# Kernel optimization log

Measured on AMD Instinct MI355X. Metric: run time of the kernel, lower is better.

The kernel has to match this reference:

```python
import jax, jax.numpy as jnp
import numpy as np

EYE_PENALTY = 1.0e6


def setup_inputs() -> dict:
    key = jax.random.key(0)
    k1, k2 = jax.random.split(key)
    B, NIN, NK, DK = 512, 1024, 128, 5
    x = jax.random.normal(k1, (B, NIN), dtype=jnp.float32)
    theta = jax.random.normal(k2, (NIN, NK, DK), dtype=jnp.float32) * 0.05
    log_weight_scale = jnp.zeros((NK, DK), dtype=jnp.float32)
    bias = jnp.full((NK,), -1.0, dtype=jnp.float32)
    return {"x": x, "theta": theta, "log_weight_scale": log_weight_scale, "bias": bias}


def reference(x, theta, log_weight_scale, bias):
    # kernel = theta * exp(log_weight_scale) / ||theta||_2 (norm over input dim)
    l2 = jnp.sqrt(jnp.sum(theta * theta, axis=0))            # [K, D]
    kernel = theta * (jnp.exp(log_weight_scale) / l2)[None]   # [NIN, K, D]
    actv = jnp.einsum('bi,ikd->bkd', x, kernel)               # [B, K, D]
    B = x.shape[0]
    # all-pairs L1 distance per kernel: [B, K, B]
    diff = actv[:, :, :, None] - jnp.transpose(actv, (1, 2, 0))[None]  # [B,K,D,B]
    abs_dif = jnp.sum(jnp.abs(diff), axis=2)                  # [B, K, B]
    abs_dif = abs_dif + EYE_PENALTY * jnp.eye(B, dtype=x.dtype)[:, None, :]
    f = jnp.sum(jnp.exp(-abs_dif), axis=2) + bias[None, :]    # [B, K]
    return jnp.concatenate([x, f], axis=1)                    # [B, NIN + K]
```

## Files before the change

### kernel.cpp

```cpp
#include <hip/hip_runtime.h>
#include <hip/hip_fp16.h>
#include <math.h>

constexpr int B    = 512;
constexpr int NIN  = 1024;
constexpr int NK   = 128;
constexpr int DK   = 5;
constexpr int NF   = NK * DK;
constexpr int NOUT = NIN + NK;
constexpr int SPLITK = 8;
constexpr int LDA = 136;
#define LOG2E 1.44269504088896f

typedef _Float16 f16x4 __attribute__((ext_vector_type(4)));
typedef _Float16 f16x8 __attribute__((ext_vector_type(8)));
typedef float    f32x4 __attribute__((ext_vector_type(4)));

union H2 { __half2 h; unsigned u; };

__global__ __launch_bounds__(256) void gemm_kernel(
        const float* __restrict__ x,
        const float* __restrict__ theta,
        __half* __restrict__ actvP16,
        float* __restrict__ ps) {
    __shared__ _Float16 Ath[32 * LDA];
    __shared__ _Float16 Bxh[64 * LDA];
    __shared__ float    red2[32][33];

    const int t    = threadIdx.x;
    const int tile = blockIdx.x >> 3;
    const int z    = blockIdx.x & 7;
    const int nt   = tile >> 3;
    const int bt   = tile & 7;
    const int n0   = nt * 32;
    const int b0   = bt * 64;
    const bool do_ps = (bt == 0);
    const int kw   = z * 128;

    const int kq = t >> 3;
    const int nc = (t & 7) * 4;
    float4 tv0 = *(const float4*)&theta[(kw + kq*4 + 0) * NF + n0 + nc];
    float4 tv1 = *(const float4*)&theta[(kw + kq*4 + 1) * NF + n0 + nc];
    float4 tv2 = *(const float4*)&theta[(kw + kq*4 + 2) * NF + n0 + nc];
    float4 tv3 = *(const float4*)&theta[(kw + kq*4 + 3) * NF + n0 + nc];

    const int br = t >> 2;
    const int ki = t & 3;
    float4 xv[8];
    #pragma unroll
    for (int i = 0; i < 8; ++i)
        xv[i] = *(const float4*)&x[(b0 + br) * NIN + kw + (ki + i * 4) * 4];

    if (do_ps) {
        red2[kq][nc + 0] = tv0.x*tv0.x + tv1.x*tv1.x + tv2.x*tv2.x + tv3.x*tv3.x;
        red2[kq][nc + 1] = tv0.y*tv0.y + tv1.y*tv1.y + tv2.y*tv2.y + tv3.y*tv3.y;
        red2[kq][nc + 2] = tv0.z*tv0.z + tv1.z*tv1.z + tv2.z*tv2.z + tv3.z*tv3.z;
        red2[kq][nc + 3] = tv0.w*tv0.w + tv1.w*tv1.w + tv2.w*tv2.w + tv3.w*tv3.w;
    }

    {
        f16x4 h;
        h[0]=(_Float16)tv0.x; h[1]=(_Float16)tv1.x; h[2]=(_Float16)tv2.x; h[3]=(_Float16)tv3.x;
        *(f16x4*)&Ath[(nc + 0) * LDA + kq * 4] = h;
        h[0]=(_Float16)tv0.y; h[1]=(_Float16)tv1.y; h[2]=(_Float16)tv2.y; h[3]=(_Float16)tv3.y;
        *(f16x4*)&Ath[(nc + 1) * LDA + kq * 4] = h;
        h[0]=(_Float16)tv0.z; h[1]=(_Float16)tv1.z; h[2]=(_Float16)tv2.z; h[3]=(_Float16)tv3.z;
        *(f16x4*)&Ath[(nc + 2) * LDA + kq * 4] = h;
        h[0]=(_Float16)tv0.w; h[1]=(_Float16)tv1.w; h[2]=(_Float16)tv2.w; h[3]=(_Float16)tv3.w;
        *(f16x4*)&Ath[(nc + 3) * LDA + kq * 4] = h;
    }
    #pragma unroll
    for (int i = 0; i < 8; ++i) {
        f16x4 h;
        h[0] = (_Float16)xv[i].x;  h[1] = (_Float16)xv[i].y;
        h[2] = (_Float16)xv[i].z;  h[3] = (_Float16)xv[i].w;
        *(f16x4*)&Bxh[br * LDA + (ki + i * 4) * 4] = h;
    }
    __syncthreads();

    const int w   = t >> 6;
    const int l   = t & 63;
    const int r16 = l & 15;
    const int kg  = l >> 4;

    f32x4 acc0 = {0.f,0.f,0.f,0.f}, acc1 = {0.f,0.f,0.f,0.f};
    #pragma unroll
    for (int ks = 0; ks < 4; ++ks) {
        const f16x8 bv  = *(const f16x8*)&Bxh[(w*16 + r16)*LDA + ks*32 + kg*8];
        const f16x8 av0 = *(const f16x8*)&Ath[( 0 + r16)*LDA + ks*32 + kg*8];
        const f16x8 av1 = *(const f16x8*)&Ath[(16 + r16)*LDA + ks*32 + kg*8];
        acc0 = __builtin_amdgcn_mfma_f32_16x16x32_f16(av0, bv, acc0, 0, 0, 0);
        acc1 = __builtin_amdgcn_mfma_f32_16x16x32_f16(av1, bv, acc1, 0, 0, 0);
    }

    {
        __half* dst = actvP16 + (size_t)z * NF * B
                    + (size_t)(n0 + kg*4) * B + b0 + w*16 + r16;
        #pragma unroll
        for (int j = 0; j < 4; ++j) {
            dst[j*B]          = __float2half(acc0[j]);
            dst[(16 + j) * B] = __float2half(acc1[j]);
        }
    }
    if (do_ps) {
        __syncthreads();
        if (t < 32) {
            float tot = 0.f;
            #pragma unroll
            for (int rr = 0; rr < 32; ++rr) tot += red2[rr][t];
            ps[z * NF + n0 + t] = tot;
        }
    }
}

__global__ __launch_bounds__(512) void pairwise_kernel(
        const __half* __restrict__ actvP16,
        const float* __restrict__ ps,
        const float* __restrict__ lws,
        const float* __restrict__ bias,
        const float* __restrict__ x,
        float* __restrict__ out) {
    __shared__ __half a16s[DK * B];
    __shared__ float  red[8 * 128];
    __shared__ float  s_sh[DK];
    __shared__ float  red_ps[DK * SPLITK];

    const int k = blockIdx.x;
    const int e = blockIdx.y;
    const int t = threadIdx.x;

    if (t >= 256) {
        const int u = t - 256;
        const int row = k * 4 + e;
        ((float4*)out)[row * (NOUT/4) + u] = ((const float4*)x)[row * (NIN/4) + u];
    }
    if (t >= 448 && t < 448 + DK * SPLITK) {
        const int u = t - 448;
        red_ps[u] = ps[(u / DK) * NF + k * DK + (u % DK)];
    }

    const size_t slab = (size_t)k * DK * B;
    float accf[8];
    #pragma unroll
    for (int i = 0; i < 8; ++i) accf[i] = 0.f;
    if (t < 320) {
        #pragma unroll
        for (int z = 0; z < SPLITK; ++z) {
            const f16x8 v = *(const f16x8*)(actvP16 + (size_t)z * NF * B + slab + t * 8);
            #pragma unroll
            for (int i = 0; i < 8; ++i) accf[i] += (float)v[i];
        }
    }
    __syncthreads();
    if (t < DK) {
        float sum = 0.f;
        #pragma unroll
        for (int c = 0; c < SPLITK; ++c) sum += red_ps[c * DK + t];
        s_sh[t] = __expf(lws[k * DK + t]) * rsqrtf(sum) * LOG2E;
    }
    __syncthreads();
    if (t < 320) {
        const float s = s_sh[t >> 6];
        f16x8 h;
        #pragma unroll
        for (int i = 0; i < 8; ++i) h[i] = (_Float16)(accf[i] * s);
        *(f16x8*)&a16s[t * 8] = h;
    }
    __syncthreads();

    const int g  = t >> 6;
    const int r  = t & 63;
    const int ba = e * 128 + r;
    const int bb = ba + 64;

    __half2 A2[DK], B2[DK];
    #pragma unroll
    for (int d = 0; d < DK; ++d) {
        A2[d] = __half2half2(a16s[d * B + ba]);
        B2[d] = __half2half2(a16s[d * B + bb]);
    }

    float accA = 0.f, accB = 0.f;
    const int bp0 = g * 64;

    union W8 { f16x8 v; __half2 h[4]; };
    typedef _Float16 f16x2v __attribute__((ext_vector_type(2)));
    union HV { __half2 h; f16x2v v; };
    const HV ones = {__half2half2(__float2half(1.0f))};

    #pragma unroll 2
    for (int m = 0; m < 8; ++m) {
        const int bp = bp0 + m * 8;
        W8 w0, w1, w2, w3, w4;
        w0.v = *(const f16x8*)&a16s[0*B + bp];
        w1.v = *(const f16x8*)&a16s[1*B + bp];
        w2.v = *(const f16x8*)&a16s[2*B + bp];
        w3.v = *(const f16x8*)&a16s[3*B + bp];
        w4.v = *(const f16x8*)&a16s[4*B + bp];
        #pragma unroll
        for (int c = 0; c < 4; ++c) {
            __half2 dA = __habs2(__hsub2(A2[0], w0.h[c]));
            dA = __hadd2(dA, __habs2(__hsub2(A2[1], w1.h[c])));
            dA = __hadd2(dA, __habs2(__hsub2(A2[2], w2.h[c])));
            dA = __hadd2(dA, __habs2(__hsub2(A2[3], w3.h[c])));
            dA = __hadd2(dA, __habs2(__hsub2(A2[4], w4.h[c])));
            HV eA; eA.h = h2exp2(__hneg2(dA));
            __half2 dB = __habs2(__hsub2(B2[0], w0.h[c]));
            dB = __hadd2(dB, __habs2(__hsub2(B2[1], w1.h[c])));
            dB = __hadd2(dB, __habs2(__hsub2(B2[2], w2.h[c])));
            dB = __hadd2(dB, __habs2(__hsub2(B2[3], w3.h[c])));
            dB = __hadd2(dB, __habs2(__hsub2(B2[4], w4.h[c])));
            HV eB; eB.h = h2exp2(__hneg2(dB));
#if __has_builtin(__builtin_amdgcn_fdot2)
            accA = __builtin_amdgcn_fdot2(eA.v, ones.v, accA, false);
            accB = __builtin_amdgcn_fdot2(eB.v, ones.v, accB, false);
#else
            accA += __low2float(eA.h) + __high2float(eA.h);
            accB += __low2float(eB.h) + __high2float(eB.h);
#endif
        }
    }
    red[g * 128 + r]      = accA;
    red[g * 128 + 64 + r] = accB;
    __syncthreads();
    if (t < 128) {
        float f = -1.0f + bias[k];
        #pragma unroll
        for (int gg = 0; gg < 8; ++gg) f += red[gg * 128 + t];
        out[(e * 128 + t) * NOUT + NIN + k] = f;
    }
}

extern "C" void kernel_launch(void* const* d_in, const int* in_sizes, int n_in,
                              void* d_out, int out_size, void* d_ws, size_t ws_size,
                              hipStream_t stream) {
    const float* x     = (const float*)d_in[0];
    const float* theta = (const float*)d_in[1];
    const float* lws   = (const float*)d_in[2];
    const float* bias  = (const float*)d_in[3];
    float* out = (float*)d_out;

    char* wsb = (char*)d_ws;
    float*  ps       = (float*)wsb;
    __half* actvP16  = (__half*)(wsb + (64 << 10));

    gemm_kernel<<<dim3(1280), 256, 0, stream>>>(x, theta, actvP16, ps);
    pairwise_kernel<<<dim3(NK, 4), 512, 0, stream>>>(actvP16, ps, lws, bias, x, out);
}
```

Baseline: 24.00 us.

## Fuse GEMM and pairwise stages into one per-kernel-slot block

```diff
diff --git a/kernel.cpp b/kernel.cpp
--- a/kernel.cpp
+++ b/kernel.cpp
@@ -6,228 +6,179 @@
 constexpr int NIN  = 1024;
 constexpr int NK   = 128;
 constexpr int DK   = 5;
-constexpr int NF   = NK * DK;
-constexpr int NOUT = NIN + NK;
-constexpr int SPLITK = 8;
-constexpr int LDA = 136;
+constexpr int NF   = 640;
+constexpr int NOUT = 1152;
+constexpr int LDB  = 40;
+constexpr int LDA  = 1040;
 #define LOG2E 1.44269504088896f
 
 typedef _Float16 f16x4 __attribute__((ext_vector_type(4)));
 typedef _Float16 f16x8 __attribute__((ext_vector_type(8)));
 typedef float    f32x4 __attribute__((ext_vector_type(4)));
 
-union H2 { __half2 h; unsigned u; };
-
-__global__ __launch_bounds__(256) void gemm_kernel(
+__global__ __launch_bounds__(1024) void fused_kernel(
         const float* __restrict__ x,
         const float* __restrict__ theta,
-        __half* __restrict__ actvP16,
-        float* __restrict__ ps) {
-    __shared__ _Float16 Ath[32 * LDA];
-    __shared__ _Float16 Bxh[64 * LDA];
-    __shared__ float    red2[32][33];
+        const float* __restrict__ lws,
+        const float* __restrict__ bias,
+        float* __restrict__ out) {
+    __shared__ __align__(16) _Float16 Ath[DK * LDA];
+    __shared__ __align__(16) _Float16 Bxh[2][512 * LDB];
+    __shared__ float wred[16][DK];
+    __shared__ float s_sh[DK];
 
-    const int t    = threadIdx.x;
-    const int tile = blockIdx.x >> 3;
-    const int z    = blockIdx.x & 7;
-    const int nt   = tile >> 3;
-    const int bt   = tile & 7;
-    const int n0   = nt * 32;
-    const int b0   = bt * 64;
-    const bool do_ps = (bt == 0);
-    const int kw   = z * 128;
+    __half* a16s = (__half*)&Ath[0];
+    float*  red  = (float*)((char*)&Ath[0] + 5376);
 
-    const int kq = t >> 3;
-    const int nc = (t & 7) * 4;
-    float4 tv0 = *(const float4*)&theta[(kw + kq*4 + 0) * NF + n0 + nc];
-    float4 tv1 = *(const float4*)&theta[(kw + kq*4 + 1) * NF + n0 + nc];
-    float4 tv2 = *(const float4*)&theta[(kw + kq*4 + 2) * NF + n0 + nc];
-    float4 tv3 = *(const float4*)&theta[(kw + kq*4 + 3) * NF + n0 + nc];
+    const int t = threadIdx.x;
+    const int k = blockIdx.x;
 
-    const int br = t >> 2;
-    const int ki = t & 3;
-    float4 xv[8];
-    #pragma unroll
-    for (int i = 0; i < 8; ++i)
-        xv[i] = *(const float4*)&x[(b0 + br) * NIN + kw + (ki + i * 4) * 4];
-
-    if (do_ps) {
-        red2[kq][nc + 0] = tv0.x*tv0.x + tv1.x*tv1.x + tv2.x*tv2.x + tv3.x*tv3.x;
-        red2[kq][nc + 1] = tv0.y*tv0.y + tv1.y*tv1.y + tv2.y*tv2.y + tv3.y*tv3.y;
-        red2[kq][nc + 2] = tv0.z*tv0.z + tv1.z*tv1.z + tv2.z*tv2.z + tv3.z*tv3.z;
-        red2[kq][nc + 3] = tv0.w*tv0.w + tv1.w*tv1.w + tv2.w*tv2.w + tv3.w*tv3.w;
+    {
+        const int row = 4 * k + (t >> 8);
+        const int c4  = t & 255;
+        ((float4*)out)[row * (NOUT / 4) + c4] =
+            ((const float4*)x)[row * (NIN / 4) + c4];
     }
 
     {
-        f16x4 h;
-        h[0]=(_Float16)tv0.x; h[1]=(_Float16)tv1.x; h[2]=(_Float16)tv2.x; h[3]=(_Float16)tv3.x;
-        *(f16x4*)&Ath[(nc + 0) * LDA + kq * 4] = h;
-        h[0]=(_Float16)tv0.y; h[1]=(_Float16)tv1.y; h[2]=(_Float16)tv2.y; h[3]=(_Float16)tv3.y;
-        *(f16x4*)&Ath[(nc + 1) * LDA + kq * 4] = h;
-        h[0]=(_Float16)tv0.z; h[1]=(_Float16)tv1.z; h[2]=(_Float16)tv2.z; h[3]=(_Float16)tv3.z;
-        *(f16x4*)&Ath[(nc + 2) * LDA + kq * 4] = h;
-        h[0]=(_Float16)tv0.w; h[1]=(_Float16)tv1.w; h[2]=(_Float16)tv2.w; h[3]=(_Float16)tv3.w;
-        *(f16x4*)&Ath[(nc + 3) * LDA + kq * 4] = h;
+        const float* tp = theta + (size_t)t * NF + k * DK;
+        float th[DK], sq[DK];
+        #pragma unroll
+        for (int d = 0; d < DK; ++d) { th[d] = tp[d]; sq[d] = th[d] * th[d]; }
+        #pragma unroll
+        for (int d = 0; d < DK; ++d) Ath[d * LDA + t] = (_Float16)th[d];
+        #pragma unroll
+        for (int d = 0; d < DK; ++d) {
+            #pragma unroll
+            for (int m = 32; m >= 1; m >>= 1) sq[d] += __shfl_xor(sq[d], m, 64);
+        }
+        if ((t & 63) == 0) {
+            #pragma unroll
+            for (int d = 0; d < DK; ++d) wred[t >> 6][d] = sq[d];
+        }
     }
-    #pragma unroll
-    for (int i = 0; i < 8; ++i) {
-        f16x4 h;
-        h[0] = (_Float16)xv[i].x;  h[1] = (_Float16)xv[i].y;
-        h[2] = (_Float16)xv[i].z;  h[3] = (_Float16)xv[i].w;
-        *(f16x4*)&Bxh[br * LDA + (ki + i * 4) * 4] = h;
+
+    {
+        const int f4i = t & 7;
+        #pragma unroll
+        for (int p = 0; p < 4; ++p) {
+            const int row = (t >> 3) + p * 128;
+            const float4 v = *(const float4*)&x[(size_t)row * NIN + f4i * 4];
+            f16x4 h;
+            h[0] = (_Float16)v.x; h[1] = (_Float16)v.y;
+            h[2] = (_Float16)v.z; h[3] = (_Float16)v.w;
+            *(f16x4*)&Bxh[0][row * LDB + f4i * 4] = h;
+        }
     }
     __syncthreads();
 
-    const int w   = t >> 6;
+    if (t < DK) {
+        float nrm = 0.f;
+        #pragma unroll
+        for (int w = 0; w < 16; ++w) nrm += wred[w][t];
+        s_sh[t] = __expf(lws[k * DK + t]) * rsqrtf(nrm) * LOG2E;
+    }
+
+    const int wv  = t >> 6;
     const int l   = t & 63;
     const int r16 = l & 15;
     const int kg  = l >> 4;
 
-    f32x4 acc0 = {0.f,0.f,0.f,0.f}, acc1 = {0.f,0.f,0.f,0.f};
-    #pragma unroll
-    for (int ks = 0; ks < 4; ++ks) {
-        const f16x8 bv  = *(const f16x8*)&Bxh[(w*16 + r16)*LDA + ks*32 + kg*8];
-        const f16x8 av0 = *(const f16x8*)&Ath[( 0 + r16)*LDA + ks*32 + kg*8];
-        const f16x8 av1 = *(const f16x8*)&Ath[(16 + r16)*LDA + ks*32 + kg*8];
-        acc0 = __builtin_amdgcn_mfma_f32_16x16x32_f16(av0, bv, acc0, 0, 0, 0);
-        acc1 = __builtin_amdgcn_mfma_f32_16x16x32_f16(av1, bv, acc1, 0, 0, 0);
+    f32x4 acc0 = {0.f, 0.f, 0.f, 0.f};
+    f32x4 acc1 = {0.f, 0.f, 0.f, 0.f};
+
+    for (int c = 0; c < 32; ++c) {
+        float4 nx[4];
+        if (c < 31) {
+            const int f4i = t & 7;
+            #pragma unroll
+            for (int p = 0; p < 4; ++p) {
+                const int row = (t >> 3) + p * 128;
+                nx[p] = *(const float4*)&x[(size_t)row * NIN + (c + 1) * 32 + f4i * 4];
+            }
+        }
+        {
+            f16x8 av = {0, 0, 0, 0, 0, 0, 0, 0};
+            if (r16 < DK)
+                av = *(const f16x8*)&Ath[r16 * LDA + c * 32 + kg * 8];
+            const f16x8 bv0 = *(const f16x8*)&Bxh[c & 1][(wv * 32      + r16) * LDB + kg * 8];
+            const f16x8 bv1 = *(const f16x8*)&Bxh[c & 1][(wv * 32 + 16 + r16) * LDB + kg * 8];
+            acc0 = __builtin_amdgcn_mfma_f32_16x16x32_f16(av, bv0, acc0, 0, 0, 0);
+            acc1 = __builtin_amdgcn_mfma_f32_16x16x32_f16(av, bv1, acc1, 0, 0, 0);
+        }
+        __syncthreads();
+        if (c < 31) {
+            const int f4i = t & 7;
+            #pragma unroll
+            for (int p = 0; p < 4; ++p) {
+                const int row = (t >> 3) + p * 128;
+                f16x4 h;
+                h[0] = (_Float16)nx[p].x; h[1] = (_Float16)nx[p].y;
+                h[2] = (_Float16)nx[p].z; h[3] = (_Float16)nx[p].w;
+                *(f16x4*)&Bxh[(c + 1) & 1][row * LDB + f4i * 4] = h;
+            }
+        }
+        __syncthreads();
     }
 
     {
-        __half* dst = actvP16 + (size_t)z * NF * B
-                    + (size_t)(n0 + kg*4) * B + b0 + w*16 + r16;
-        #pragma unroll
-        for (int j = 0; j < 4; ++j) {
-            dst[j*B]          = __float2half(acc0[j]);
-            dst[(16 + j) * B] = __float2half(acc1[j]);
-        }
-    }
-    if (do_ps) {
-        __syncthreads();
-        if (t < 32) {
-            float tot = 0.f;
+        const int c0 = wv * 32 + r16;
+        if (kg == 0) {
             #pragma unroll
-            for (int rr = 0; rr < 32; ++rr) tot += red2[rr][t];
-            ps[z * NF + n0 + t] = tot;
-        }
-    }
-}
-
-__global__ __launch_bounds__(512) void pairwise_kernel(
-        const __half* __restrict__ actvP16,
-        const float* __restrict__ ps,
-        const float* __restrict__ lws,
-        const float* __restrict__ bias,
-        const float* __restrict__ x,
-        float* __restrict__ out) {
-    __shared__ __half a16s[DK * B];
-    __shared__ float  red[8 * 128];
-    __shared__ float  s_sh[DK];
-    __shared__ float  red_ps[DK * SPLITK];
-
-    const int k = blockIdx.x;
-    const int e = blockIdx.y;
-    const int t = threadIdx.x;
-
-    if (t >= 256) {
-        const int u = t - 256;
-        const int row = k * 4 + e;
-        ((float4*)out)[row * (NOUT/4) + u] = ((const float4*)x)[row * (NIN/4) + u];
-    }
-    if (t >= 448 && t < 448 + DK * SPLITK) {
-        const int u = t - 448;
-        red_ps[u] = ps[(u / DK) * NF + k * DK + (u % DK)];
-    }
-
-    const size_t slab = (size_t)k * DK * B;
-    float accf[8];
-    #pragma unroll
-    for (int i = 0; i < 8; ++i) accf[i] = 0.f;
-    if (t < 320) {
-        #pragma unroll
-        for (int z = 0; z < SPLITK; ++z) {
-            const f16x8 v = *(const f16x8*)(actvP16 + (size_t)z * NF * B + slab + t * 8);
-            #pragma unroll
-            for (int i = 0; i < 8; ++i) accf[i] += (float)v[i];
+            for (int j = 0; j < 4; ++j) {
+                a16s[j * B + c0]      = __float2half(acc0[j] * s_sh[j]);
+                a16s[j * B + c0 + 16] = __float2half(acc1[j] * s_sh[j]);
+            }
+        } else if (kg == 1) {
+            a16s[4 * B + c0]      = __float2half(acc0[0] * s_sh[4]);
+            a16s[4 * B + c0 + 16] = __float2half(acc1[0] * s_sh[4]);
         }
     }
     __syncthreads();
-    if (t < DK) {
-        float sum = 0.f;
-        #pragma unroll
-        for (int c = 0; c < SPLITK; ++c) sum += red_ps[c * DK + t];
-        s_sh[t] = __expf(lws[k * DK + t]) * rsqrtf(sum) * LOG2E;
-    }
-    __syncthreads();
-    if (t < 320) {
-        const float s = s_sh[t >> 6];
-        f16x8 h;
-        #pragma unroll
-        for (int i = 0; i < 8; ++i) h[i] = (_Float16)(accf[i] * s);
-        *(f16x8*)&a16s[t * 8] = h;
-    }
-    __syncthreads();
 
-    const int g  = t >> 6;
-    const int r  = t & 63;
-    const int ba = e * 128 + r;
-    const int bb = ba + 64;
+    const int b = t & 511;
+    const int h = t >> 9;
 
-    __half2 A2[DK], B2[DK];
+    __half2 A2[DK];
     #pragma unroll
-    for (int d = 0; d < DK; ++d) {
-        A2[d] = __half2half2(a16s[d * B + ba]);
-        B2[d] = __half2half2(a16s[d * B + bb]);
-    }
+    for (int d = 0; d < DK; ++d) A2[d] = __half2half2(a16s[d * B + b]);
 
-    float accA = 0.f, accB = 0.f;
-    const int bp0 = g * 64;
-
-    union W8 { f16x8 v; __half2 h[4]; };
     typedef _Float16 f16x2v __attribute__((ext_vector_type(2)));
     union HV { __half2 h; f16x2v v; };
+    union W8 { f16x8 v; __half2 h[4]; };
     const HV ones = {__half2half2(__float2half(1.0f))};
 
+    float acc = 0.f;
+    const int bp0 = h * 256;
     #pragma unroll 2
-    for (int m = 0; m < 8; ++m) {
+    for (int m = 0; m < 32; ++m) {
         const int bp = bp0 + m * 8;
         W8 w0, w1, w2, w3, w4;
-        w0.v = *(const f16x8*)&a16s[0*B + bp];
-        w1.v = *(const f16x8*)&a16s[1*B + bp];
-        w2.v = *(const f16x8*)&a16s[2*B + bp];
-        w3.v = *(const f16x8*)&a16s[3*B + bp];
-        w4.v = *(const f16x8*)&a16s[4*B + bp];
+        w0.v = *(const f16x8*)(a16s + 0 * B + bp);
+        w1.v = *(const f16x8*)(a16s + 1 * B + bp);
+        w2.v = *(const f16x8*)(a16s + 2 * B + bp);
+        w3.v = *(const f16x8*)(a16s + 3 * B + bp);
+        w4.v = *(const f16x8*)(a16s + 4 * B + bp);
         #pragma unroll
-        for (int c = 0; c < 4; ++c) {
-            __half2 dA = __habs2(__hsub2(A2[0], w0.h[c]));
-            dA = __hadd2(dA, __habs2(__hsub2(A2[1], w1.h[c])));
-            dA = __hadd2(dA, __habs2(__hsub2(A2[2], w2.h[c])));
-            dA = __hadd2(dA, __habs2(__hsub2(A2[3], w3.h[c])));
-            dA = __hadd2(dA, __habs2(__hsub2(A2[4], w4.h[c])));
+        for (int cc = 0; cc < 4; ++cc) {
+            __half2 dA = __habs2(__hsub2(A2[0], w0.h[cc]));
+            dA = __hadd2(dA, __habs2(__hsub2(A2[1], w1.h[cc])));
+            dA = __hadd2(dA, __habs2(__hsub2(A2[2], w2.h[cc])));
+            dA = __hadd2(dA, __habs2(__hsub2(A2[3], w3.h[cc])));
+            dA = __hadd2(dA, __habs2(__hsub2(A2[4], w4.h[cc])));
             HV eA; eA.h = h2exp2(__hneg2(dA));
-            __half2 dB = __habs2(__hsub2(B2[0], w0.h[c]));
-            dB = __hadd2(dB, __habs2(__hsub2(B2[1], w1.h[c])));
-            dB = __hadd2(dB, __habs2(__hsub2(B2[2], w2.h[c])));
-            dB = __hadd2(dB, __habs2(__hsub2(B2[3], w3.h[c])));
-            dB = __hadd2(dB, __habs2(__hsub2(B2[4], w4.h[c])));
-            HV eB; eB.h = h2exp2(__hneg2(dB));
 #if __has_builtin(__builtin_amdgcn_fdot2)
-            accA = __builtin_amdgcn_fdot2(eA.v, ones.v, accA, false);
-            accB = __builtin_amdgcn_fdot2(eB.v, ones.v, accB, false);
+            acc = __builtin_amdgcn_fdot2(eA.v, ones.v, acc, false);
 #else
-            accA += __low2float(eA.h) + __high2float(eA.h);
-            accB += __low2float(eB.h) + __high2float(eB.h);
+            acc += __low2float(eA.h) + __high2float(eA.h);
 #endif
         }
     }
-    red[g * 128 + r]      = accA;
-    red[g * 128 + 64 + r] = accB;
+    red[h * B + b] = acc;
     __syncthreads();
-    if (t < 128) {
-        float f = -1.0f + bias[k];
-        #pragma unroll
-        for (int gg = 0; gg < 8; ++gg) f += red[gg * 128 + t];
-        out[(e * 128 + t) * NOUT + NIN + k] = f;
+    if (t < B) {
+        const float f = red[t] + red[B + t] - 1.0f + bias[k];
+        out[(size_t)t * NOUT + NIN + k] = f;
     }
 }
 
@@ -240,10 +191,5 @@
     const float* bias  = (const float*)d_in[3];
     float* out = (float*)d_out;
 
-    char* wsb = (char*)d_ws;
-    float*  ps       = (float*)wsb;
-    __half* actvP16  = (__half*)(wsb + (64 << 10));
-
-    gemm_kernel<<<dim3(1280), 256, 0, stream>>>(x, theta, actvP16, ps);
-    pairwise_kernel<<<dim3(NK, 4), 512, 0, stream>>>(actvP16, ps, lws, bias, x, out);
+    fused_kernel<<<dim3(NK), 1024, 0, stream>>>(x, theta, lws, bias, out);
 }
```

Measured after the change: 64.97 us. 171% more time.

## Split split-K reduction into separate kernel and widen pairwise grid

Applied to the files above, without the earlier changes.

```diff
diff --git a/kernel.cpp b/kernel.cpp
--- a/kernel.cpp
+++ b/kernel.cpp
@@ -15,8 +15,6 @@
 typedef _Float16 f16x4 __attribute__((ext_vector_type(4)));
 typedef _Float16 f16x8 __attribute__((ext_vector_type(8)));
 typedef float    f32x4 __attribute__((ext_vector_type(4)));
-
-union H2 { __half2 h; unsigned u; };
 
 __global__ __launch_bounds__(256) void gemm_kernel(
         const float* __restrict__ x,
@@ -113,83 +111,74 @@
     }
 }
 
-__global__ __launch_bounds__(512) void pairwise_kernel(
+__global__ __launch_bounds__(256) void rs_kernel(
         const __half* __restrict__ actvP16,
         const float* __restrict__ ps,
         const float* __restrict__ lws,
+        __half* __restrict__ a16) {
+    const int u   = blockIdx.x * 256 + threadIdx.x;
+    const int row = u >> 6;
+    const int c8  = (u & 63) * 8;
+
+    float nrm = 0.f;
+    #pragma unroll
+    for (int z = 0; z < SPLITK; ++z) nrm += ps[z * NF + row];
+    const float s = __expf(lws[row]) * rsqrtf(nrm) * LOG2E;
+
+    float accf[8];
+    #pragma unroll
+    for (int i = 0; i < 8; ++i) accf[i] = 0.f;
+    const __half* p = actvP16 + (size_t)row * B + c8;
+    #pragma unroll
+    for (int z = 0; z < SPLITK; ++z) {
+        const f16x8 v = *(const f16x8*)(p + (size_t)z * NF * B);
+        #pragma unroll
+        for (int i = 0; i < 8; ++i) accf[i] += (float)v[i];
+    }
+    f16x8 h;
+    #pragma unroll
+    for (int i = 0; i < 8; ++i) h[i] = (_Float16)(accf[i] * s);
+    *(f16x8*)&a16[(size_t)row * B + c8] = h;
+}
+
+__global__ __launch_bounds__(256) void pairwise_kernel(
+        const __half* __restrict__ a16,
         const float* __restrict__ bias,
         const float* __restrict__ x,
         float* __restrict__ out) {
     __shared__ __half a16s[DK * B];
-    __shared__ float  red[8 * 128];
-    __shared__ float  s_sh[DK];
-    __shared__ float  red_ps[DK * SPLITK];
+    __shared__ float  red[4 * 64];
 
     const int k = blockIdx.x;
     const int e = blockIdx.y;
     const int t = threadIdx.x;
 
-    if (t >= 256) {
-        const int u = t - 256;
+    if (e < 4) {
         const int row = k * 4 + e;
-        ((float4*)out)[row * (NOUT/4) + u] = ((const float4*)x)[row * (NIN/4) + u];
-    }
-    if (t >= 448 && t < 448 + DK * SPLITK) {
-        const int u = t - 448;
-        red_ps[u] = ps[(u / DK) * NF + k * DK + (u % DK)];
-    }
-
-    const size_t slab = (size_t)k * DK * B;
-    float accf[8];
-    #pragma unroll
-    for (int i = 0; i < 8; ++i) accf[i] = 0.f;
-    if (t < 320) {
-        #pragma unroll
-        for (int z = 0; z < SPLITK; ++z) {
-            const f16x8 v = *(const f16x8*)(actvP16 + (size_t)z * NF * B + slab + t * 8);
-            #pragma unroll
-            for (int i = 0; i < 8; ++i) accf[i] += (float)v[i];
-        }
-    }
-    __syncthreads();
-    if (t < DK) {
-        float sum = 0.f;
-        #pragma unroll
-        for (int c = 0; c < SPLITK; ++c) sum += red_ps[c * DK + t];
-        s_sh[t] = __expf(lws[k * DK + t]) * rsqrtf(sum) * LOG2E;
-    }
-    __syncthreads();
-    if (t < 320) {
-        const float s = s_sh[t >> 6];
-        f16x8 h;
-        #pragma unroll
-        for (int i = 0; i < 8; ++i) h[i] = (_Float16)(accf[i] * s);
-        *(f16x8*)&a16s[t * 8] = h;
+        ((float4*)out)[row * (NOUT/4) + t] = ((const float4*)x)[row * (NIN/4) + t];
+    }
+
+    {
+        const uint4* src = (const uint4*)(a16 + (size_t)k * DK * B);
+        ((uint4*)a16s)[t] = src[t];
+        if (t < 64) ((uint4*)a16s)[256 + t] = src[256 + t];
     }
     __syncthreads();
 
     const int g  = t >> 6;
     const int r  = t & 63;
-    const int ba = e * 128 + r;
-    const int bb = ba + 64;
-
-    __half2 A2[DK], B2[DK];
-    #pragma unroll
-    for (int d = 0; d < DK; ++d) {
-        A2[d] = __half2half2(a16s[d * B + ba]);
-        B2[d] = __half2half2(a16s[d * B + bb]);
-    }
-
-    float accA = 0.f, accB = 0.f;
-    const int bp0 = g * 64;
+    const int ba = e * 64 + r;
+
+    __half2 A2[DK];
+    #pragma unroll
+    for (int d = 0; d < DK; ++d) A2[d] = __half2half2(a16s[d * B + ba]);
 
     union W8 { f16x8 v; __half2 h[4]; };
-    typedef _Float16 f16x2v __attribute__((ext_vector_type(2)));
-    union HV { __half2 h; f16x2v v; };
-    const HV ones = {__half2half2(__float2half(1.0f))};
-
+
+    float acc = 0.f;
+    const int bp0 = g * 128;
     #pragma unroll 2
-    for (int m = 0; m < 8; ++m) {
+    for (int m = 0; m < 16; ++m) {
         const int bp = bp0 + m * 8;
         W8 w0, w1, w2, w3, w4;
         w0.v = *(const f16x8*)&a16s[0*B + bp];
@@ -204,30 +193,18 @@
             dA = __hadd2(dA, __habs2(__hsub2(A2[2], w2.h[c])));
             dA = __hadd2(dA, __habs2(__hsub2(A2[3], w3.h[c])));
             dA = __hadd2(dA, __habs2(__hsub2(A2[4], w4.h[c])));
-            HV eA; eA.h = h2exp2(__hneg2(dA));
-            __half2 dB = __habs2(__hsub2(B2[0], w0.h[c]));
-            dB = __hadd2(dB, __habs2(__hsub2(B2[1], w1.h[c])));
-            dB = __hadd2(dB, __habs2(__hsub2(B2[2], w2.h[c])));
-            dB = __hadd2(dB, __habs2(__hsub2(B2[3], w3.h[c])));
-            dB = __hadd2(dB, __habs2(__hsub2(B2[4], w4.h[c])));
-            HV eB; eB.h = h2exp2(__hneg2(dB));
-#if __has_builtin(__builtin_amdgcn_fdot2)
-            accA = __builtin_amdgcn_fdot2(eA.v, ones.v, accA, false);
-            accB = __builtin_amdgcn_fdot2(eB.v, ones.v, accB, false);
-#else
-            accA += __low2float(eA.h) + __high2float(eA.h);
-            accB += __low2float(eB.h) + __high2float(eB.h);
-#endif
+            const float lo = __low2float(dA);
+            const float hi = __high2float(dA);
+            acc += __builtin_amdgcn_exp2f(-lo);
+            acc += __builtin_amdgcn_exp2f(-hi);
         }
     }
-    red[g * 128 + r]      = accA;
-    red[g * 128 + 64 + r] = accB;
+    red[g * 64 + r] = acc;
     __syncthreads();
-    if (t < 128) {
-        float f = -1.0f + bias[k];
-        #pragma unroll
-        for (int gg = 0; gg < 8; ++gg) f += red[gg * 128 + t];
-        out[(e * 128 + t) * NOUT + NIN + k] = f;
+    if (t < 64) {
+        const float f = ((red[t] + red[64 + t]) + (red[128 + t] + red[192 + t]))
+                        - 1.0f + bias[k];
+        out[(e * 64 + t) * NOUT + NIN + k] = f;
     }
 }
 
@@ -241,9 +218,11 @@
     float* out = (float*)d_out;
 
     char* wsb = (char*)d_ws;
-    float*  ps       = (float*)wsb;
-    __half* actvP16  = (__half*)(wsb + (64 << 10));
+    float*  ps      = (float*)wsb;
+    __half* actvP16 = (__half*)(wsb + (64 << 10));
+    __half* a16     = (__half*)(wsb + (64 << 10) + (size_t)SPLITK * 2 * NF * B);
 
     gemm_kernel<<<dim3(1280), 256, 0, stream>>>(x, theta, actvP16, ps);
-    pairwise_kernel<<<dim3(NK, 4), 512, 0, stream>>>(actvP16, ps, lws, bias, x, out);
-}
+    rs_kernel<<<dim3(160), 256, 0, stream>>>(actvP16, ps, lws, a16);
+    pairwise_kernel<<<dim3(NK, 8), 256, 0, stream>>>(a16, bias, x, out);
+}
```

Result: slower. 26.79 us (+11.6%).
